# Optimization experiments

Hardware: AMD Instinct MI355X
Metric: run time of the kernel (lower is better)

Reference implementation:

```python
import jax, jax.numpy as jnp
import numpy as np

N, T, D, H1, H2, NH = 4096, 2048, 256, 128, 32, 4
ALPHA = 0.2  # LeakyReLU slope in GAT
NEG = -9e15  # mask value for non-edges


def _gat(x, adj, W, a_src, a_dst, fc_W, fc_b):
    # Multi-head GAT (pygat style), heads stacked on leading axis, then Linear fc.
    Wh = jnp.einsum('nd,hde->hne', x, W)                    # [NH, n, d_out]
    f = jnp.einsum('hne,he->hn', Wh, a_src)                 # a^T [Wh_i || .]
    g = jnp.einsum('hne,he->hn', Wh, a_dst)                 # a^T [. || Wh_j]
    e = jax.nn.leaky_relu(f[:, :, None] + g[:, None, :], ALPHA)  # [NH, n, n]
    e = jnp.where(adj[None, :, :] > 0, e, NEG)
    att = jax.nn.softmax(e, axis=-1)
    h = jax.nn.elu(jnp.einsum('hnm,hme->hne', att, Wh))     # concat=True -> ELU
    h = jnp.transpose(h, (1, 0, 2)).reshape(x.shape[0], -1)  # [n, NH*d_out]
    return h @ fc_W + fc_b


def setup_inputs() -> dict:
    key = jax.random.key(0)
    ks = jax.random.split(key, 24)
    s = 0.1
    x = jax.random.normal(ks[0], (N, D), jnp.float32)
    t_x = jax.random.normal(ks[1], (T, D), jnp.float32)
    adj = (jax.random.uniform(ks[2], (N, N)) < 0.005).astype(jnp.float32) + jnp.eye(N, dtype=jnp.float32)
    t_adj = (jax.random.uniform(ks[3], (T, T)) < 0.01).astype(jnp.float32) + jnp.eye(T, dtype=jnp.float32)
    tfidf_x = jax.random.uniform(ks[4], (T, N), jnp.float32) * 0.01
    p = lambda k, shp: jax.random.normal(k, shp, jnp.float32) * s
    return {
        'x': x, 'adj': adj, 't_x': t_x, 't_adj': t_adj, 'tfidf_x': tfidf_x,
        # concept-graph MHGAT (in D -> per-head D, concat NH*D -> fc -> D)
        'gat_W': p(ks[5], (NH, D, D)), 'gat_asrc': p(ks[6], (NH, D)), 'gat_adst': p(ks[7], (NH, D)),
        'gat_fcW': p(ks[8], (NH * D, D)), 'gat_fcb': jnp.zeros((D,), jnp.float32),
        # text-graph MHGAT
        't_W': p(ks[9], (NH, D, D)), 't_asrc': p(ks[10], (NH, D)), 't_adst': p(ks[11], (NH, D)),
        't_fcW': p(ks[12], (NH * D, D)), 't_fcb': jnp.zeros((D,), jnp.float32),
        # gated fusion fc
        'fus_W': p(ks[13], (D, D)), 'fus_b': jnp.zeros((D,), jnp.float32),
        # GCN encoder weights (Kipf VGAE GraphConvolution: adj @ (x @ W))
        'gc1_W': p(ks[14], (D, H1)), 'gc2_W': p(ks[15], (H1, H2)), 'gc3_W': p(ks[16], (H1, H2)),
    }


def reference(x, adj, t_x, t_adj, tfidf_x,
              gat_W, gat_asrc, gat_adst, gat_fcW, gat_fcb,
              t_W, t_asrc, t_adst, t_fcW, t_fcb,
              fus_W, fus_b, gc1_W, gc2_W, gc3_W):
    # gated fusion of concept-graph and text-graph GAT outputs (eval mode, dropout off)
    concept = _gat(x, adj, gat_W, gat_asrc, gat_adst, gat_fcW, gat_fcb)      # [N, D]
    gat_text = _gat(t_x, t_adj, t_W, t_asrc, t_adst, t_fcW, t_fcb)           # [T, D]
    c_text = tfidf_x.T @ gat_text                                            # [N, D]
    z = jax.nn.sigmoid(concept + c_text)
    fusion = (z * concept + (1.0 - z) * c_text) @ fus_W + fus_b              # [N, D]
    # GCN VAE encoder
    h1 = jax.nn.relu(adj @ (fusion @ gc1_W))                                 # [N, H1]
    mu = adj @ (h1 @ gc2_W)                                                  # [N, H2]
    logvar = adj @ (h1 @ gc3_W)                                              # [N, H2]
    # eval-mode reparameterize -> z_lat = mu; decoder act is identity in GCNModelVAE
    recon = mu @ mu.T                                                        # [N, N]
    return recon, mu, logvar
```

## Files before the change

kernel.cpp:

```cpp
#include <hip/hip_runtime.h>
#include <hip/hip_bf16.h>

#define MAX_E 128
typedef __attribute__((ext_vector_type(8))) short bf16x8;
typedef __attribute__((ext_vector_type(4))) float f32x4;

__device__ __forceinline__ unsigned short f2bf(float f) {
    union { float f; unsigned u; } a; a.f = f;
    unsigned r = a.u + 0x7FFFu + ((a.u >> 16) & 1u);
    return (unsigned short)(r >> 16);
}
__device__ __forceinline__ float bf2f(unsigned short s) {
    union { unsigned u; float f; } a; a.u = ((unsigned)s) << 16; return a.f;
}
__device__ __forceinline__ float wave_sum(float v) {
#pragma unroll
    for (int o = 1; o < 64; o <<= 1) v += __shfl_xor(v, o, 64);
    return v;
}
__device__ __forceinline__ float wave_max(float v) {
#pragma unroll
    for (int o = 1; o < 64; o <<= 1) v = fmaxf(v, __shfl_xor(v, o, 64));
    return v;
}

#define MAXJ 16
struct TJobs {
    const float* src[MAXJ];
    unsigned short* dst[MAXJ];
    int R[MAXJ], C[MAXJ], tb[MAXJ];
    int njobs;
};

__global__ __launch_bounds__(256) void prep_k(
        const float* __restrict__ adj, const float* __restrict__ t_adj,
        int* __restrict__ cnt, int* __restrict__ eidx_c, int* __restrict__ eidx_t,
        const float* __restrict__ gat_W, const float* __restrict__ gat_asrc,
        const float* __restrict__ gat_adst, const float* __restrict__ t_W,
        const float* __restrict__ t_asrc, const float* __restrict__ t_adst,
        float* __restrict__ APDP, TJobs tj) {
    __shared__ float smem[1056];
    int bid = blockIdx.x, tid = threadIdx.x;
    if (bid < 6144) {
        int* s_cnt = (int*)smem;
        if (tid == 0) *s_cnt = 0;
        __syncthreads();
        if (bid < 4096) {
            const float4* ar = (const float4*)(adj + (size_t)bid * 4096);
            int* er = eidx_c + (size_t)bid * MAX_E;
#pragma unroll
            for (int it = 0; it < 4; it++) {
                float4 v = ar[tid + it * 256];
                int jb = (tid + it * 256) * 4;
#pragma unroll
                for (int c = 0; c < 4; c++) {
                    float vv = c == 0 ? v.x : c == 1 ? v.y : c == 2 ? v.z : v.w;
                    if (vv > 0.f) {
                        int p = atomicAdd(s_cnt, 1);
                        if (p < MAX_E) er[p] = (jb + c) | (vv > 1.5f ? 0x40000000 : 0);
                    }
                }
            }
        } else {
            int r = bid - 4096;
            const float4* ar = (const float4*)(t_adj + (size_t)r * 2048);
            int* er = eidx_t + (size_t)r * MAX_E;
#pragma unroll
            for (int it = 0; it < 2; it++) {
                float4 v = ar[tid + it * 256];
                int jb = (tid + it * 256) * 4;
#pragma unroll
                for (int c = 0; c < 4; c++) {
                    float vv = c == 0 ? v.x : c == 1 ? v.y : c == 2 ? v.z : v.w;
                    if (vv > 0.f) {
                        int p = atomicAdd(s_cnt, 1);
                        if (p < MAX_E) er[p] = jb + c;
                    }
                }
            }
        }
        __syncthreads();
        if (tid == 0) cnt[bid] = *s_cnt < MAX_E ? *s_cnt : MAX_E;
    } else if (bid < 6152) {
        int pb = bid - 6144, h = pb & 3, g = pb >> 2, d = tid;
        const float* W  = g ? t_W : gat_W;
        const float* as = g ? t_asrc : gat_asrc;
        const float* ad = g ? t_adst : gat_adst;
        float* sa = smem; float* sd = smem + 256;
        sa[d] = as[h * 256 + d]; sd[d] = ad[h * 256 + d];
        __syncthreads();
        const float* wr = W + (size_t)h * 65536 + (size_t)d * 256;
        float ap = 0.f, dp = 0.f;
        for (int e = 0; e < 256; e++) { float w = wr[e]; ap += w * sa[e]; dp += w * sd[e]; }
        APDP[g * 1024 + h * 256 + d] = ap;
        APDP[2048 + g * 1024 + h * 256 + d] = dp;
    } else {
        int local = bid - 6152;
        int j = 0;
        while (j + 1 < tj.njobs && local >= tj.tb[j + 1]) j++;
        local -= tj.tb[j];
        int R = tj.R[j], C = tj.C[j];
        int xt = C >> 5;
        int tx = local % xt, ty = local / xt;
        const float* in = tj.src[j];
        unsigned short* outp = tj.dst[j];
        float (*t)[33] = (float(*)[33])smem;
        int jj = tid & 31, ii = tid >> 5;
        int r0 = ty * 32, c0 = tx * 32;
#pragma unroll
        for (int k = 0; k < 4; k++) { int rl = ii + k * 8; t[rl][jj] = in[(size_t)(r0 + rl) * C + c0 + jj]; }
        __syncthreads();
#pragma unroll
        for (int k = 0; k < 4; k++) { int cl = ii + k * 8; outp[(size_t)(c0 + cl) * R + r0 + jj] = f2bf(t[jj][cl]); }
    }
}

__global__ __launch_bounds__(256) void whfg_k(
        const float* __restrict__ x, const float* __restrict__ t_x,
        const unsigned short* __restrict__ WT, const unsigned short* __restrict__ TWT,
        unsigned short* __restrict__ WHC, unsigned short* __restrict__ WHT,
        const float* __restrict__ APDP, float* __restrict__ FC, float* __restrict__ GC,
        float* __restrict__ FT, float* __restrict__ GT) {
    __shared__ __align__(16) unsigned short As[64 * 40], Bs[64 * 40];
    int bid = blockIdx.x, tid = threadIdx.x;
    if (bid < 1536) {
        int g, xk, y, h;
        if (bid < 1024) { g = 0; xk = bid & 3; y = (bid >> 2) & 63; h = bid >> 8; }
        else { int b2 = bid - 1024; g = 1; xk = b2 & 3; y = (b2 >> 2) & 31; h = b2 >> 7; }
        const float* Af = g ? t_x : x;
        const unsigned short* Bt = (g ? TWT : WT) + h * 65536;
        unsigned short* C = (g ? WHT : WHC) + h * 256;
        int m0 = y * 64, n0 = xk * 64;
        int wave = tid >> 6, lane = tid & 63, quad = lane >> 4, r = lane & 15;
        int lrow = tid >> 2, lcol8 = (tid & 3) * 8;
        f32x4 acc[4] = {{0.f,0.f,0.f,0.f},{0.f,0.f,0.f,0.f},{0.f,0.f,0.f,0.f},{0.f,0.f,0.f,0.f}};
        for (int k0 = 0; k0 < 256; k0 += 32) {
            const float* ap = Af + (size_t)(m0 + lrow) * 256 + k0 + lcol8;
            float4 a0 = *(const float4*)ap;
            float4 a1 = *(const float4*)(ap + 4);
            ushort4 u0 = {f2bf(a0.x), f2bf(a0.y), f2bf(a0.z), f2bf(a0.w)};
            ushort4 u1 = {f2bf(a1.x), f2bf(a1.y), f2bf(a1.z), f2bf(a1.w)};
            uint4 bv = *(const uint4*)(Bt + (size_t)(n0 + lrow) * 256 + k0 + lcol8);
            *(ushort4*)(&As[lrow * 40 + lcol8]) = u0;
            *(ushort4*)(&As[lrow * 40 + lcol8 + 4]) = u1;
            *(uint4*)(&Bs[lrow * 40 + lcol8]) = bv;
            __syncthreads();
            bf16x8 af = *(const bf16x8*)(&As[(wave * 16 + r) * 40 + quad * 8]);
#pragma unroll
            for (int nj = 0; nj < 4; nj++) {
                bf16x8 bfr = *(const bf16x8*)(&Bs[(nj * 16 + r) * 40 + quad * 8]);
                acc[nj] = __builtin_amdgcn_mfma_f32_16x16x32_bf16(af, bfr, acc[nj], 0, 0, 0);
            }
            __syncthreads();
        }
#pragma unroll
        for (int nj = 0; nj < 4; nj++) {
            int n = n0 + nj * 16 + r;
#pragma unroll
            for (int reg = 0; reg < 4; reg++) {
                int m = m0 + wave * 16 + quad * 4 + reg;
                C[(size_t)m * 1024 + n] = f2bf(acc[nj][reg]);
            }
        }
    } else {
        int b = bid - 1536;
        int h = tid >> 6, lane = tid & 63;
        const float* xr; float* F; float* G; const float* AP; const float* DP; int n, i;
        if (b < 4096) { i = b; xr = x + (size_t)i * 256; F = FC; G = GC; AP = APDP; DP = APDP + 2048; n = 4096; }
        else { i = b - 4096; xr = t_x + (size_t)i * 256; F = FT; G = GT; AP = APDP + 1024; DP = APDP + 3072; n = 2048; }
        float vf = 0.f, vg = 0.f;
#pragma unroll
        for (int c = 0; c < 4; c++) {
            int d = c * 64 + lane;
            float xv = xr[d];
            vf += xv * AP[h * 256 + d];
            vg += xv * DP[h * 256 + d];
        }
        vf = wave_sum(vf); vg = wave_sum(vg);
        if (lane == 0) { F[h * n + i] = vf; G[h * n + i] = vg; }
    }
}

__global__ __launch_bounds__(256) void agg_all_k(const unsigned short* __restrict__ WHC,
        const unsigned short* __restrict__ WHT, const float* __restrict__ FC,
        const float* __restrict__ GC, const float* __restrict__ FT,
        const float* __restrict__ GT, const int* __restrict__ cnt,
        const int* __restrict__ eidx_c, const int* __restrict__ eidx_t,
        unsigned short* __restrict__ HCC, unsigned short* __restrict__ HCT) {
    int b = blockIdx.x, tid = threadIdx.x;
    int h = tid >> 6, lane = tid & 63;
    int ne = cnt[b];
    const unsigned short* WH; const float* F; const float* G; const int* ei;
    unsigned short* HC; int n, i;
    if (b < 4096) { i = b; n = 4096; WH = WHC; F = FC; G = GC; ei = eidx_c + (size_t)i * MAX_E; HC = HCC; }
    else { i = b - 4096; n = 2048; WH = WHT; F = FT; G = GT; ei = eidx_t + (size_t)i * MAX_E; HC = HCT; }
    __shared__ int s_col[MAX_E];
    __shared__ float s_w[4][MAX_E];
    for (int e = tid; e < ne; e += 256) s_col[e] = ei[e] & 0xFFFF;
    __syncthreads();
    float fi = F[h * n + i];
    float lmax = -1e30f;
    for (int e = lane; e < ne; e += 64) {
        float xv = fi + G[h * n + s_col[e]];
        xv = xv >= 0.f ? xv : 0.2f * xv;
        s_w[h][e] = xv;
        lmax = fmaxf(lmax, xv);
    }
    lmax = wave_max(lmax);
    float lsum = 0.f;
    for (int e = lane; e < ne; e += 64) {
        float w = __expf(s_w[h][e] - lmax);
        s_w[h][e] = w;
        lsum += w;
    }
    lsum = wave_sum(lsum);
    float inv = 1.f / lsum;
    float a0 = 0.f, a1 = 0.f, a2 = 0.f, a3 = 0.f;
    const unsigned short* base = WH + h * 256 + lane * 4;
    for (int e = 0; e < ne; e++) {
        float w = s_w[h][e];
        ushort4 q = *(const ushort4*)(base + (size_t)s_col[e] * 1024);
        a0 += w * bf2f(q.x); a1 += w * bf2f(q.y); a2 += w * bf2f(q.z); a3 += w * bf2f(q.w);
    }
    a0 *= inv; a1 *= inv; a2 *= inv; a3 *= inv;
    a0 = a0 > 0.f ? a0 : __expf(a0) - 1.f;
    a1 = a1 > 0.f ? a1 : __expf(a1) - 1.f;
    a2 = a2 > 0.f ? a2 : __expf(a2) - 1.f;
    a3 = a3 > 0.f ? a3 : __expf(a3) - 1.f;
    ushort4 st; st.x = f2bf(a0); st.y = f2bf(a1); st.z = f2bf(a2); st.w = f2bf(a3);
    *(ushort4*)(HC + (size_t)i * 1024 + h * 256 + lane * 4) = st;
}

__device__ __forceinline__ void mfma_core(const unsigned short* __restrict__ A,
        const unsigned short* __restrict__ Bt, int K, int m0, int n0,
        unsigned short* As, unsigned short* Bs, f32x4 acc[4]) {
    int tid = threadIdx.x;
    int wave = tid >> 6, lane = tid & 63, quad = lane >> 4, r = lane & 15;
    int lrow = tid >> 2, lcol8 = (tid & 3) * 8;
    for (int k0 = 0; k0 < K; k0 += 32) {
        uint4 av = *(const uint4*)(A + (size_t)(m0 + lrow) * K + k0 + lcol8);
        uint4 bv = *(const uint4*)(Bt + (size_t)(n0 + lrow) * K + k0 + lcol8);
        *(uint4*)(&As[lrow * 40 + lcol8]) = av;
        *(uint4*)(&Bs[lrow * 40 + lcol8]) = bv;
        __syncthreads();
        bf16x8 af = *(const bf16x8*)(&As[(wave * 16 + r) * 40 + quad * 8]);
#pragma unroll
        for (int nj = 0; nj < 4; nj++) {
            bf16x8 bfr = *(const bf16x8*)(&Bs[(nj * 16 + r) * 40 + quad * 8]);
            acc[nj] = __builtin_amdgcn_mfma_f32_16x16x32_bf16(af, bfr, acc[nj], 0, 0, 0);
        }
        __syncthreads();
    }
}

__global__ __launch_bounds__(256) void fc_both_k(const unsigned short* __restrict__ HCC,
        const unsigned short* __restrict__ HCT, const unsigned short* __restrict__ FCWT,
        const unsigned short* __restrict__ TFCWT, const float* __restrict__ fcb,
        const float* __restrict__ tfcb, float* __restrict__ CPT,
        unsigned short* __restrict__ GTT) {
    __shared__ __align__(16) unsigned short As[64 * 40], Bs[64 * 40];
    int z = blockIdx.z;
    int M = z ? 2048 : 4096;
    int m0 = blockIdx.y * 64, n0 = blockIdx.x * 64;
    if (m0 >= M) return;
    const unsigned short* A = z ? HCT : HCC;
    const unsigned short* Bt = z ? TFCWT : FCWT;
    const float* bias = z ? tfcb : fcb;
    f32x4 acc[4] = {{0.f,0.f,0.f,0.f},{0.f,0.f,0.f,0.f},{0.f,0.f,0.f,0.f},{0.f,0.f,0.f,0.f}};
    mfma_core(A, Bt, 1024, m0, n0, As, Bs, acc);
    int tid = threadIdx.x, wave = tid >> 6, lane = tid & 63, quad = lane >> 4, r = lane & 15;
#pragma unroll
    for (int nj = 0; nj < 4; nj++) {
        int n = n0 + nj * 16 + r;
        float bv = bias[n];
        if (z == 0) {
#pragma unroll
            for (int reg = 0; reg < 4; reg++) {
                int m = m0 + wave * 16 + quad * 4 + reg;
                CPT[(size_t)m * 256 + n] = acc[nj][reg] + bv;
            }
        } else {
            int mb = m0 + wave * 16 + quad * 4;
            ushort4 st;
            st.x = f2bf(acc[nj][0] + bv); st.y = f2bf(acc[nj][1] + bv);
            st.z = f2bf(acc[nj][2] + bv); st.w = f2bf(acc[nj][3] + bv);
            *(ushort4*)(GTT + (size_t)n * 2048 + mb) = st;
        }
    }
}

template <int EP>
__global__ __launch_bounds__(256) void gemm_ep_k(const unsigned short* __restrict__ A,
        const unsigned short* __restrict__ Bt, const float* __restrict__ bias,
        const float* __restrict__ aux, void* __restrict__ Cv,
        int M, int N, int K, int ldc) {
    __shared__ __align__(16) unsigned short As[64 * 40], Bs[64 * 40];
    int m0 = blockIdx.y * 64, n0 = blockIdx.x * 64;
    if (m0 >= M) return;
    f32x4 acc[4] = {{0.f,0.f,0.f,0.f},{0.f,0.f,0.f,0.f},{0.f,0.f,0.f,0.f},{0.f,0.f,0.f,0.f}};
    mfma_core(A, Bt, K, m0, n0, As, Bs, acc);
    int tid = threadIdx.x, wave = tid >> 6, lane = tid & 63, quad = lane >> 4, r = lane & 15;
#pragma unroll
    for (int nj = 0; nj < 4; nj++) {
        int n = n0 + nj * 16 + r;
        float bv = (EP == 2) ? bias[n] : 0.f;
#pragma unroll
        for (int reg = 0; reg < 4; reg++) {
            int m = m0 + wave * 16 + quad * 4 + reg;
            float v = acc[nj][reg] + bv;
            if (EP == 0) ((float*)Cv)[(size_t)m * ldc + n] = v;
            else if (EP == 2) ((unsigned short*)Cv)[(size_t)m * ldc + n] = f2bf(v);
            else {
                float c = aux[(size_t)m * ldc + n];
                float z = 1.f / (1.f + __expf(-(c + v)));
                ((unsigned short*)Cv)[(size_t)m * ldc + n] = f2bf(z * c + (1.f - z) * v);
            }
        }
    }
}

__global__ void spmm_h1_k(const int* __restrict__ cnt, const int* __restrict__ eidx,
                          const float* __restrict__ T1, unsigned short* __restrict__ H1B) {
    int i = blockIdx.x, tid = threadIdx.x;
    int ne = cnt[i];
    __shared__ int s_e[MAX_E];
    for (int e = tid; e < ne; e += 128) s_e[e] = eidx[(size_t)i * MAX_E + e];
    __syncthreads();
    float acc = 0.f;
    for (int e = 0; e < ne; e++) {
        int p = s_e[e];
        float v = (p & 0x40000000) ? 2.f : 1.f;
        acc += v * T1[(size_t)(p & 0xFFFF) * 128 + tid];
    }
    H1B[(size_t)i * 128 + tid] = f2bf(fmaxf(acc, 0.f));
}

__global__ void spmm_mu_k(const int* __restrict__ cnt, const int* __restrict__ eidx,
                          const unsigned short* __restrict__ H1B,
                          const unsigned short* __restrict__ GC23WT,
                          float* __restrict__ MU, float* __restrict__ LOGVAR,
                          unsigned short* __restrict__ MUBF) {
    int i = blockIdx.x, tid = threadIdx.x;
    int ne = cnt[i];
    __shared__ int s_e[MAX_E];
    __shared__ float s_a2[128];
    for (int e = tid; e < ne; e += 128) s_e[e] = eidx[(size_t)i * MAX_E + e];
    __syncthreads();
    float acc = 0.f;
    for (int e = 0; e < ne; e++) {
        int p = s_e[e];
        float v = (p & 0x40000000) ? 2.f : 1.f;
        acc += v * bf2f(H1B[(size_t)(p & 0xFFFF) * 128 + tid]);
    }
    s_a2[tid] = acc;
    __syncthreads();
    if (tid < 64) {
        const unsigned short* w = GC23WT + tid * 128;
        float o = 0.f;
        for (int k = 0; k < 128; k++) o += s_a2[k] * bf2f(w[k]);
        if (tid < 32) { MU[(size_t)i * 32 + tid] = o; MUBF[(size_t)i * 32 + tid] = f2bf(o); }
        else LOGVAR[(size_t)i * 32 + (tid - 32)] = o;
    }
}

extern "C" void kernel_launch(void* const* d_in, const int* in_sizes, int n_in,
                              void* d_out, int out_size, void* d_ws, size_t ws_size,
                              hipStream_t stream) {
    const float* x        = (const float*)d_in[0];
    const float* adj      = (const float*)d_in[1];
    const float* t_x      = (const float*)d_in[2];
    const float* t_adj    = (const float*)d_in[3];
    const float* tfidf    = (const float*)d_in[4];
    const float* gat_W    = (const float*)d_in[5];
    const float* gat_asrc = (const float*)d_in[6];
    const float* gat_adst = (const float*)d_in[7];
    const float* gat_fcW  = (const float*)d_in[8];
    const float* gat_fcb  = (const float*)d_in[9];
    const float* t_W      = (const float*)d_in[10];
    const float* t_asrc   = (const float*)d_in[11];
    const float* t_adst   = (const float*)d_in[12];
    const float* t_fcW    = (const float*)d_in[13];
    const float* t_fcb    = (const float*)d_in[14];
    const float* fus_W    = (const float*)d_in[15];
    const float* fus_b    = (const float*)d_in[16];
    const float* gc1_W    = (const float*)d_in[17];
    const float* gc2_W    = (const float*)d_in[18];
    const float* gc3_W    = (const float*)d_in[19];

    float* out = (float*)d_out;
    float* ws  = (float*)d_ws;

    unsigned short* WHC   = (unsigned short*)(ws + 0);
    unsigned short* HCC   = (unsigned short*)(ws + 2097152);
    unsigned short* WHT   = (unsigned short*)(ws + 4194304);
    unsigned short* HCT   = (unsigned short*)(ws + 5242880);
    unsigned short* TFT   = (unsigned short*)(ws + 6291456);
    unsigned short* FUSION= (unsigned short*)(ws + 6291456);
    unsigned short* MUBF  = (unsigned short*)(ws + 6815744);
    float* CPT            = ws + 10485760;
    unsigned short* GTT   = (unsigned short*)(ws + 11534336);
    unsigned short* FUSEIN= (unsigned short*)(ws + 11796480);
    float* T1             = ws + 12320768;
    unsigned short* H1B   = (unsigned short*)(ws + 12845056);
    float* FC             = ws + 13107200;
    float* GC             = ws + 13123584;
    float* FT             = ws + 13139968;
    float* GT             = ws + 13148160;
    float* APDP           = ws + 13156352;
    unsigned short* WT    = (unsigned short*)(ws + 13160448);
    unsigned short* TWT   = (unsigned short*)(ws + 13291520);
    unsigned short* FCWT  = (unsigned short*)(ws + 13422592);
    unsigned short* TFCWT = (unsigned short*)(ws + 13553664);
    unsigned short* FUSWT = (unsigned short*)(ws + 13684736);
    unsigned short* GC1WT = (unsigned short*)(ws + 13717504);
    unsigned short* GC23WT= (unsigned short*)(ws + 13733888);
    int* ECNT             = (int*)(ws + 13737984);
    int* EIDX_C           = (int*)(ws + 13744128);
    int* EIDX_T           = (int*)(ws + 14268416);
    float* MU     = out + (size_t)4096 * 4096;
    float* LOGVAR = MU + (size_t)4096 * 32;

    TJobs tj = {};
    int nj = 0, tb = 0;
    auto add = [&](const float* s, unsigned short* d, int R, int C) {
        tj.src[nj] = s; tj.dst[nj] = d; tj.R[nj] = R; tj.C[nj] = C; tj.tb[nj] = tb;
        tb += (R >> 5) * (C >> 5); nj++;
    };
    for (int h = 0; h < 4; h++) add(gat_W + h * 65536, WT + h * 65536, 256, 256);
    for (int h = 0; h < 4; h++) add(t_W + h * 65536, TWT + h * 65536, 256, 256);
    add(gat_fcW, FCWT, 1024, 256);
    add(t_fcW, TFCWT, 1024, 256);
    add(fus_W, FUSWT, 256, 256);
    add(gc1_W, GC1WT, 256, 128);
    add(gc2_W, GC23WT, 128, 32);
    add(gc3_W, GC23WT + 32 * 128, 128, 32);
    add(tfidf, TFT, 2048, 4096);
    tj.njobs = nj;
    prep_k<<<6152 + tb, 256, 0, stream>>>(adj, t_adj, ECNT, EIDX_C, EIDX_T,
        gat_W, gat_asrc, gat_adst, t_W, t_asrc, t_adst, APDP, tj);

    whfg_k<<<1536 + 6144, 256, 0, stream>>>(x, t_x, WT, TWT, WHC, WHT, APDP, FC, GC, FT, GT);

    agg_all_k<<<6144, 256, 0, stream>>>(WHC, WHT, FC, GC, FT, GT, ECNT, EIDX_C, EIDX_T, HCC, HCT);

    fc_both_k<<<dim3(4, 64, 2), 256, 0, stream>>>(HCC, HCT, FCWT, TFCWT, gat_fcb, t_fcb, CPT, GTT);

    gemm_ep_k<3><<<dim3(4, 64), 256, 0, stream>>>(TFT, GTT, nullptr, CPT, FUSEIN, 4096, 256, 2048, 256);

    gemm_ep_k<2><<<dim3(4, 64), 256, 0, stream>>>(FUSEIN, FUSWT, fus_b, nullptr, FUSION, 4096, 256, 256, 256);

    gemm_ep_k<0><<<dim3(2, 64), 256, 0, stream>>>(FUSION, GC1WT, nullptr, nullptr, T1, 4096, 128, 256, 128);

    spmm_h1_k<<<4096, 128, 0, stream>>>(ECNT, EIDX_C, T1, H1B);

    spmm_mu_k<<<4096, 128, 0, stream>>>(ECNT, EIDX_C, H1B, GC23WT, MU, LOGVAR, MUBF);

    gemm_ep_k<0><<<dim3(64, 64), 256, 0, stream>>>(MUBF, MUBF, nullptr, nullptr, out, 4096, 4096, 32, 4096);
}
```

Before: 330.4 us.

## Fold fus_W into gc1_W and read tfidf directly in the gated c_text GEMM

Precomputes W2 = fus_W @ gc1_W and b2 = fus_b @ gc1_W inside the prep kernel. This removes the separate fusion GEMM: T1 now comes from one GEMM of the gated input against W2. The tfidf transpose-to-bf16 job is dropped, and a new kernel loads tfidf fp32 directly, converts it in registers into swizzled LDS, and applies the sigmoid gate in its epilogue. The intent is to save one kernel launch, a GEMM, and the large tfidf transpose write and read. In exchange the new kernel does uncoalesced-ish strided fp32 loads and conversions per tile, and the folded weights are rounded to bf16 once.

```diff
diff --git a/kernel.cpp b/kernel.cpp
--- a/kernel.cpp
+++ b/kernel.cpp
@@ -38,8 +38,11 @@
         const float* __restrict__ gat_W, const float* __restrict__ gat_asrc,
         const float* __restrict__ gat_adst, const float* __restrict__ t_W,
         const float* __restrict__ t_asrc, const float* __restrict__ t_adst,
-        float* __restrict__ APDP, TJobs tj) {
-    __shared__ float smem[1056];
+        float* __restrict__ APDP,
+        const float* __restrict__ fus_W, const float* __restrict__ fus_b,
+        const float* __restrict__ gc1_W, unsigned short* __restrict__ W2T,
+        float* __restrict__ B2, int w2_base, TJobs tj) {
+    __shared__ float smem[2080];
     int bid = blockIdx.x, tid = threadIdx.x;
     if (bid < 6144) {
         int* s_cnt = (int*)smem;
@@ -48,13 +51,15 @@
         if (bid < 4096) {
             const float4* ar = (const float4*)(adj + (size_t)bid * 4096);
             int* er = eidx_c + (size_t)bid * MAX_E;
+            float4 v0 = ar[tid], v1 = ar[tid + 256], v2 = ar[tid + 512], v3 = ar[tid + 768];
+            float va[16] = {v0.x, v0.y, v0.z, v0.w, v1.x, v1.y, v1.z, v1.w,
+                            v2.x, v2.y, v2.z, v2.w, v3.x, v3.y, v3.z, v3.w};
 #pragma unroll
             for (int it = 0; it < 4; it++) {
-                float4 v = ar[tid + it * 256];
                 int jb = (tid + it * 256) * 4;
 #pragma unroll
                 for (int c = 0; c < 4; c++) {
-                    float vv = c == 0 ? v.x : c == 1 ? v.y : c == 2 ? v.z : v.w;
+                    float vv = va[it * 4 + c];
                     if (vv > 0.f) {
                         int p = atomicAdd(s_cnt, 1);
                         if (p < MAX_E) er[p] = (jb + c) | (vv > 1.5f ? 0x40000000 : 0);
@@ -65,14 +70,14 @@
             int r = bid - 4096;
             const float4* ar = (const float4*)(t_adj + (size_t)r * 2048);
             int* er = eidx_t + (size_t)r * MAX_E;
+            float4 v0 = ar[tid], v1 = ar[tid + 256];
+            float va[8] = {v0.x, v0.y, v0.z, v0.w, v1.x, v1.y, v1.z, v1.w};
 #pragma unroll
             for (int it = 0; it < 2; it++) {
-                float4 v = ar[tid + it * 256];
                 int jb = (tid + it * 256) * 4;
 #pragma unroll
                 for (int c = 0; c < 4; c++) {
-                    float vv = c == 0 ? v.x : c == 1 ? v.y : c == 2 ? v.z : v.w;
-                    if (vv > 0.f) {
+                    if (va[it * 4 + c] > 0.f) {
                         int p = atomicAdd(s_cnt, 1);
                         if (p < MAX_E) er[p] = jb + c;
                     }
@@ -94,7 +99,7 @@
         for (int e = 0; e < 256; e++) { float w = wr[e]; ap += w * sa[e]; dp += w * sd[e]; }
         APDP[g * 1024 + h * 256 + d] = ap;
         APDP[2048 + g * 1024 + h * 256 + d] = dp;
-    } else {
+    } else if (bid < w2_base) {
         int local = bid - 6152;
         int j = 0;
         while (j + 1 < tj.njobs && local >= tj.tb[j + 1]) j++;
@@ -112,6 +117,34 @@
         __syncthreads();
 #pragma unroll
         for (int k = 0; k < 4; k++) { int cl = ii + k * 8; outp[(size_t)(c0 + cl) * R + r0 + jj] = f2bf(t[jj][cl]); }
+    } else if (bid < w2_base + 32) {
+        int bW = bid - w2_base;
+        int n0 = (bW & 3) * 32, k0 = (bW >> 2) * 32;
+        int nn = tid & 31, kb = (tid >> 5) * 4;
+        float (*s_a)[65] = (float(*)[65])smem;
+        float acc[4] = {0.f, 0.f, 0.f, 0.f};
+        for (int ec = 0; ec < 4; ec++) {
+            for (int t = tid; t < 32 * 64; t += 256) {
+                int kk2 = t >> 6, ee = t & 63;
+                s_a[kk2][ee] = fus_W[(size_t)(k0 + kk2) * 256 + ec * 64 + ee];
+            }
+            __syncthreads();
+            for (int ee = 0; ee < 64; ee++) {
+                float b = gc1_W[(size_t)(ec * 64 + ee) * 128 + n0 + nn];
+#pragma unroll
+                for (int c = 0; c < 4; c++) acc[c] += s_a[kb + c][ee] * b;
+            }
+            __syncthreads();
+        }
+#pragma unroll
+        for (int c = 0; c < 4; c++)
+            W2T[(size_t)(n0 + nn) * 256 + k0 + kb + c] = f2bf(acc[c]);
+    } else {
+        if (tid < 128) {
+            float acc = 0.f;
+            for (int k = 0; k < 256; k++) acc += fus_b[k] * gc1_W[(size_t)k * 128 + tid];
+            B2[tid] = acc;
+        }
     }
 }
 
@@ -289,11 +322,59 @@
     }
 }
 
+__global__ __launch_bounds__(256) void ctext_gate_k(
+        const float* __restrict__ tfidf, const unsigned short* __restrict__ GTT,
+        const float* __restrict__ CPT, unsigned short* __restrict__ FUSEIN) {
+    __shared__ __align__(16) unsigned short As[64 * 40], Bs[64 * 40];
+    int tid = threadIdx.x;
+    int wave = tid >> 6, lane = tid & 63, quad = lane >> 4, r = lane & 15;
+    int m0 = blockIdx.y * 64, n0 = blockIdx.x * 64;
+    int kk = tid >> 3;
+    int jj = tid & 7;
+    int b  = kk >> 3, t7 = kk & 7;
+    int lrow = tid >> 2, lcol8 = (tid & 3) * 8;
+    int mfr = wave * 16 + r;
+    int cswz = (mfr >> 3) & 3;
+    f32x4 acc[4] = {{0.f,0.f,0.f,0.f},{0.f,0.f,0.f,0.f},{0.f,0.f,0.f,0.f},{0.f,0.f,0.f,0.f}};
+    for (int k0 = 0; k0 < 2048; k0 += 32) {
+        const float* ap = tfidf + (size_t)(k0 + kk) * 4096 + m0 + jj * 8;
+        float4 a0 = *(const float4*)ap;
+        float4 a1 = *(const float4*)(ap + 4);
+        uint4 bv = *(const uint4*)(GTT + (size_t)(n0 + lrow) * 2048 + k0 + lcol8);
+        float av[8] = {a0.x, a0.y, a0.z, a0.w, a1.x, a1.y, a1.z, a1.w};
+#pragma unroll
+        for (int i = 0; i < 8; i++) {
+            int m = jj * 8 + i;
+            As[m * 40 + ((b ^ (jj & 3)) * 8) + t7] = f2bf(av[i]);
+        }
+        *(uint4*)(&Bs[lrow * 40 + lcol8]) = bv;
+        __syncthreads();
+        bf16x8 af = *(const bf16x8*)(&As[mfr * 40 + ((quad ^ cswz) * 8)]);
+#pragma unroll
+        for (int nj = 0; nj < 4; nj++) {
+            bf16x8 bfr = *(const bf16x8*)(&Bs[(nj * 16 + r) * 40 + quad * 8]);
+            acc[nj] = __builtin_amdgcn_mfma_f32_16x16x32_bf16(af, bfr, acc[nj], 0, 0, 0);
+        }
+        __syncthreads();
+    }
+#pragma unroll
+    for (int nj = 0; nj < 4; nj++) {
+        int n = n0 + nj * 16 + r;
+#pragma unroll
+        for (int reg = 0; reg < 4; reg++) {
+            int m = m0 + wave * 16 + quad * 4 + reg;
+            float v = acc[nj][reg];
+            float c = CPT[(size_t)m * 256 + n];
+            float z = 1.f / (1.f + __expf(-(c + v)));
+            FUSEIN[(size_t)m * 256 + n] = f2bf(z * c + (1.f - z) * v);
+        }
+    }
+}
+
 template <int EP>
 __global__ __launch_bounds__(256) void gemm_ep_k(const unsigned short* __restrict__ A,
         const unsigned short* __restrict__ Bt, const float* __restrict__ bias,
-        const float* __restrict__ aux, void* __restrict__ Cv,
-        int M, int N, int K, int ldc) {
+        void* __restrict__ Cv, int M, int N, int K, int ldc) {
     __shared__ __align__(16) unsigned short As[64 * 40], Bs[64 * 40];
     int m0 = blockIdx.y * 64, n0 = blockIdx.x * 64;
     if (m0 >= M) return;
@@ -303,18 +384,11 @@
 #pragma unroll
     for (int nj = 0; nj < 4; nj++) {
         int n = n0 + nj * 16 + r;
-        float bv = (EP == 2) ? bias[n] : 0.f;
+        float bv = (EP == 1) ? bias[n] : 0.f;
 #pragma unroll
         for (int reg = 0; reg < 4; reg++) {
             int m = m0 + wave * 16 + quad * 4 + reg;
-            float v = acc[nj][reg] + bv;
-            if (EP == 0) ((float*)Cv)[(size_t)m * ldc + n] = v;
-            else if (EP == 2) ((unsigned short*)Cv)[(size_t)m * ldc + n] = f2bf(v);
-            else {
-                float c = aux[(size_t)m * ldc + n];
-                float z = 1.f / (1.f + __expf(-(c + v)));
-                ((unsigned short*)Cv)[(size_t)m * ldc + n] = f2bf(z * c + (1.f - z) * v);
-            }
+            ((float*)Cv)[(size_t)m * ldc + n] = acc[nj][reg] + bv;
         }
     }
 }
@@ -394,29 +468,27 @@
     unsigned short* HCC   = (unsigned short*)(ws + 2097152);
     unsigned short* WHT   = (unsigned short*)(ws + 4194304);
     unsigned short* HCT   = (unsigned short*)(ws + 5242880);
-    unsigned short* TFT   = (unsigned short*)(ws + 6291456);
-    unsigned short* FUSION= (unsigned short*)(ws + 6291456);
-    unsigned short* MUBF  = (unsigned short*)(ws + 6815744);
-    float* CPT            = ws + 10485760;
-    unsigned short* GTT   = (unsigned short*)(ws + 11534336);
-    unsigned short* FUSEIN= (unsigned short*)(ws + 11796480);
-    float* T1             = ws + 12320768;
-    unsigned short* H1B   = (unsigned short*)(ws + 12845056);
-    float* FC             = ws + 13107200;
-    float* GC             = ws + 13123584;
-    float* FT             = ws + 13139968;
-    float* GT             = ws + 13148160;
-    float* APDP           = ws + 13156352;
-    unsigned short* WT    = (unsigned short*)(ws + 13160448);
-    unsigned short* TWT   = (unsigned short*)(ws + 13291520);
-    unsigned short* FCWT  = (unsigned short*)(ws + 13422592);
-    unsigned short* TFCWT = (unsigned short*)(ws + 13553664);
-    unsigned short* FUSWT = (unsigned short*)(ws + 13684736);
-    unsigned short* GC1WT = (unsigned short*)(ws + 13717504);
-    unsigned short* GC23WT= (unsigned short*)(ws + 13733888);
-    int* ECNT             = (int*)(ws + 13737984);
-    int* EIDX_C           = (int*)(ws + 13744128);
-    int* EIDX_T           = (int*)(ws + 14268416);
+    float* CPT            = ws + 6291456;
+    unsigned short* GTT   = (unsigned short*)(ws + 7340032);
+    unsigned short* FUSEIN= (unsigned short*)(ws + 7602176);
+    float* T1             = ws + 8126464;
+    unsigned short* H1B   = (unsigned short*)(ws + 8650752);
+    unsigned short* MUBF  = (unsigned short*)(ws + 8912896);
+    float* FC             = ws + 8978432;
+    float* GC             = ws + 8994816;
+    float* FT             = ws + 9011200;
+    float* GT             = ws + 9019392;
+    float* APDP           = ws + 9027584;
+    unsigned short* WT    = (unsigned short*)(ws + 9031680);
+    unsigned short* TWT   = (unsigned short*)(ws + 9162752);
+    unsigned short* FCWT  = (unsigned short*)(ws + 9293824);
+    unsigned short* TFCWT = (unsigned short*)(ws + 9424896);
+    unsigned short* W2T   = (unsigned short*)(ws + 9555968);
+    float* B2             = ws + 9572352;
+    unsigned short* GC23WT= (unsigned short*)(ws + 9572480);
+    int* ECNT             = (int*)(ws + 9576576);
+    int* EIDX_C           = (int*)(ws + 9582720);
+    int* EIDX_T           = (int*)(ws + 10107008);
     float* MU     = out + (size_t)4096 * 4096;
     float* LOGVAR = MU + (size_t)4096 * 32;
 
@@ -430,14 +502,13 @@
     for (int h = 0; h < 4; h++) add(t_W + h * 65536, TWT + h * 65536, 256, 256);
     add(gat_fcW, FCWT, 1024, 256);
     add(t_fcW, TFCWT, 1024, 256);
-    add(fus_W, FUSWT, 256, 256);
-    add(gc1_W, GC1WT, 256, 128);
     add(gc2_W, GC23WT, 128, 32);
     add(gc3_W, GC23WT + 32 * 128, 128, 32);
-    add(tfidf, TFT, 2048, 4096);
     tj.njobs = nj;
-    prep_k<<<6152 + tb, 256, 0, stream>>>(adj, t_adj, ECNT, EIDX_C, EIDX_T,
-        gat_W, gat_asrc, gat_adst, t_W, t_asrc, t_adst, APDP, tj);
+    int w2_base = 6152 + tb;
+    prep_k<<<w2_base + 33, 256, 0, stream>>>(adj, t_adj, ECNT, EIDX_C, EIDX_T,
+        gat_W, gat_asrc, gat_adst, t_W, t_asrc, t_adst, APDP,
+        fus_W, fus_b, gc1_W, W2T, B2, w2_base, tj);
 
     whfg_k<<<1536 + 6144, 256, 0, stream>>>(x, t_x, WT, TWT, WHC, WHT, APDP, FC, GC, FT, GT);
 
@@ -445,15 +516,13 @@
 
     fc_both_k<<<dim3(4, 64, 2), 256, 0, stream>>>(HCC, HCT, FCWT, TFCWT, gat_fcb, t_fcb, CPT, GTT);
 
-    gemm_ep_k<3><<<dim3(4, 64), 256, 0, stream>>>(TFT, GTT, nullptr, CPT, FUSEIN, 4096, 256, 2048, 256);
-
-    gemm_ep_k<2><<<dim3(4, 64), 256, 0, stream>>>(FUSEIN, FUSWT, fus_b, nullptr, FUSION, 4096, 256, 256, 256);
-
-    gemm_ep_k<0><<<dim3(2, 64), 256, 0, stream>>>(FUSION, GC1WT, nullptr, nullptr, T1, 4096, 128, 256, 128);
+    ctext_gate_k<<<dim3(4, 64), 256, 0, stream>>>(tfidf, GTT, CPT, FUSEIN);
+
+    gemm_ep_k<1><<<dim3(2, 64), 256, 0, stream>>>(FUSEIN, W2T, B2, T1, 4096, 128, 256, 128);
 
     spmm_h1_k<<<4096, 128, 0, stream>>>(ECNT, EIDX_C, T1, H1B);
 
     spmm_mu_k<<<4096, 128, 0, stream>>>(ECNT, EIDX_C, H1B, GC23WT, MU, LOGVAR, MUBF);
 
-    gemm_ep_k<0><<<dim3(64, 64), 256, 0, stream>>>(MUBF, MUBF, nullptr, nullptr, out, 4096, 4096, 32, 4096);
-}
+    gemm_ep_k<0><<<dim3(64, 64), 256, 0, stream>>>(MUBF, MUBF, nullptr, out, 4096, 4096, 32, 4096);
+}
```

New measurement: 356.2 us. 1.08x slower.
